# Optimization experiments

Hardware: AMD Instinct MI355X
Metric: run time of the kernel (lower is better)

Reference implementation:

```python
import jax, jax.numpy as jnp
import numpy as np

B, S, D, H = 4, 2048, 1024, 16
DK = D // H

def setup_inputs() -> dict:
    key = jax.random.key(0)
    ks = jax.random.split(key, 11)
    s = 1.0 / np.sqrt(D)
    return {
        "query": jax.random.normal(ks[0], (B, S, D), jnp.float32),
        "key": jax.random.normal(ks[1], (B, S, D), jnp.float32),
        "value": jax.random.normal(ks[2], (B, S, D), jnp.float32),
        "Wq_w": jax.random.normal(ks[3], (D, D), jnp.float32) * s,
        "Wq_b": jnp.zeros((D,), jnp.float32),
        "Wk_w": jax.random.normal(ks[4], (D, D), jnp.float32) * s,
        "Wk_b": jnp.zeros((D,), jnp.float32),
        "Wv_w": jax.random.normal(ks[5], (D, D), jnp.float32) * s,
        "Wv_b": jnp.zeros((D,), jnp.float32),
        "Wo_w": jax.random.normal(ks[6], (D, D), jnp.float32) * s,
        "Wo_b": jnp.zeros((D,), jnp.float32),
    }

def reference(query, key, value, Wq_w, Wq_b, Wk_w, Wk_b, Wv_w, Wv_b, Wo_w, Wo_b):
    b, s, d = query.shape
    # Linear projections (torch Linear: x @ W.T + b)
    q = query @ Wq_w.T + Wq_b
    k = key @ Wk_w.T + Wk_b
    v = value @ Wv_w.T + Wv_b
    # split heads -> [B, H, S, DK]
    q = q.reshape(b, s, H, DK).transpose(0, 2, 1, 3)
    k = k.reshape(b, s, H, DK).transpose(0, 2, 1, 3)
    v = v.reshape(b, s, H, DK).transpose(0, 2, 1, 3)
    # scaled dot-product attention
    scores = jnp.einsum("bhqd,bhkd->bhqk", q, k) / jnp.sqrt(jnp.asarray(DK, q.dtype))
    attn = jax.nn.softmax(scores, axis=-1)
    z = jnp.einsum("bhqk,bhkd->bhqd", attn, v)
    # merge heads and output projection
    z = z.transpose(0, 2, 1, 3).reshape(b, s, H * DK)
    return z @ Wo_w.T + Wo_b
```

## Files before the change

kernel.cpp:

```cpp
#include <hip/hip_runtime.h>
#include <stdint.h>

typedef unsigned short u16;
typedef __bf16 bf16x8 __attribute__((ext_vector_type(8)));
typedef float f32x4 __attribute__((ext_vector_type(4)));

#define B_   4
#define S_   2048
#define D_   1024
#define H_   16
#define DK_  64
#define MTOK (B_*S_)
#define LOG2E 1.4426950408889634f

static __device__ __forceinline__ float exp2_fast(float x){
  return __builtin_amdgcn_exp2f(x);
}

static __device__ __forceinline__ void gload_lds16(const void* g, void* l){
  __builtin_amdgcn_global_load_lds(
      (const __attribute__((address_space(1))) unsigned int*)g,
      (__attribute__((address_space(3))) unsigned int*)l, 16, 0, 0);
}

union bf8pack { __bf16 h[8]; uint4 u; };

__global__ void cvt4(const float* __restrict__ s0, const float* __restrict__ s1,
                     const float* __restrict__ s2, const float* __restrict__ s3,
                     u16* __restrict__ out, int n8){
  const float* s = blockIdx.y==0 ? s0 : blockIdx.y==1 ? s1 : blockIdx.y==2 ? s2 : s3;
  u16* o = out + (size_t)blockIdx.y * ((size_t)n8 * 8);
  int i = blockIdx.x * blockDim.x + threadIdx.x;
  int stride = gridDim.x * blockDim.x;
  for (; i < n8; i += stride){
    float4 v0 = reinterpret_cast<const float4*>(s)[i*2];
    float4 v1 = reinterpret_cast<const float4*>(s)[i*2+1];
    bf8pack p;
    p.h[0]=(__bf16)v0.x; p.h[1]=(__bf16)v0.y; p.h[2]=(__bf16)v0.z; p.h[3]=(__bf16)v0.w;
    p.h[4]=(__bf16)v1.x; p.h[5]=(__bf16)v1.y; p.h[6]=(__bf16)v1.z; p.h[7]=(__bf16)v1.w;
    reinterpret_cast<uint4*>(o)[i] = p.u;
  }
}

__global__ __launch_bounds__(256) void gemm_qkv(
    const float* __restrict__ q_in, const float* __restrict__ k_in, const float* __restrict__ v_in,
    const u16* __restrict__ wq, const u16* __restrict__ wk, const u16* __restrict__ wv,
    const float* __restrict__ bq, const float* __restrict__ bk, const float* __restrict__ bv,
    u16* __restrict__ Qb, u16* __restrict__ Kb, u16* __restrict__ VtG){
  const int z = blockIdx.z;
  const float* Ap   = z==0 ? q_in : z==1 ? k_in : v_in;
  const u16*   Bw   = z==0 ? wq : z==1 ? wk : wv;
  const float* bias = z==0 ? bq : z==1 ? bk : bv;
  const float scale = z==0 ? 0.125f*LOG2E : 1.0f;
  u16* Cb = z==0 ? Qb : z==1 ? Kb : VtG;

  __shared__ u16 As[2][128][32];
  __shared__ u16 Bs[2][128][32];
  const int tid  = threadIdx.x;
  const int lane = tid & 63;
  const int wid  = tid >> 6;
  const int wr = wid >> 1, wc = wid & 1;
  const int r15 = lane & 15, q4 = lane >> 4;
  const int bm = blockIdx.x, bn = blockIdx.y;
  const int K = D_, N = D_;
  const int NT = K / 32;

  const int r = tid >> 2, c = (tid & 3) << 3;
  const float* Ar0 = Ap + (size_t)(bm*128 + r)*K + c;
  const float* Ar1 = Ap + (size_t)(bm*128 + r + 64)*K + c;
  const u16*  Br0 = Bw + (size_t)(bn*128 + r)*K + c;
  const u16*  Br1 = Bw + (size_t)(bn*128 + r + 64)*K + c;

  f32x4 acc[4][4] = {};

  {
    float4 v00 = *reinterpret_cast<const float4*>(Ar0);
    float4 v01 = *reinterpret_cast<const float4*>(Ar0 + 4);
    float4 v10 = *reinterpret_cast<const float4*>(Ar1);
    float4 v11 = *reinterpret_cast<const float4*>(Ar1 + 4);
    bf8pack p0, p1;
    p0.h[0]=(__bf16)v00.x; p0.h[1]=(__bf16)v00.y; p0.h[2]=(__bf16)v00.z; p0.h[3]=(__bf16)v00.w;
    p0.h[4]=(__bf16)v01.x; p0.h[5]=(__bf16)v01.y; p0.h[6]=(__bf16)v01.z; p0.h[7]=(__bf16)v01.w;
    p1.h[0]=(__bf16)v10.x; p1.h[1]=(__bf16)v10.y; p1.h[2]=(__bf16)v10.z; p1.h[3]=(__bf16)v10.w;
    p1.h[4]=(__bf16)v11.x; p1.h[5]=(__bf16)v11.y; p1.h[6]=(__bf16)v11.z; p1.h[7]=(__bf16)v11.w;
    *reinterpret_cast<uint4*>(&As[0][r][c])    = p0.u;
    *reinterpret_cast<uint4*>(&As[0][r+64][c]) = p1.u;
    gload_lds16(Br0, &Bs[0][r][c]);
    gload_lds16(Br1, &Bs[0][r+64][c]);
  }
  __syncthreads();

  for (int t = 0; t < NT; ++t){
    const int cur = t & 1;
    float4 v00, v01, v10, v11;
    const bool pf = (t + 1 < NT);
    if (pf){
      const float* p0 = Ar0 + (t+1)*32;
      const float* p1 = Ar1 + (t+1)*32;
      v00 = *reinterpret_cast<const float4*>(p0);
      v01 = *reinterpret_cast<const float4*>(p0 + 4);
      v10 = *reinterpret_cast<const float4*>(p1);
      v11 = *reinterpret_cast<const float4*>(p1 + 4);
      gload_lds16(Br0 + (t+1)*32, &Bs[cur^1][r][c]);
      gload_lds16(Br1 + (t+1)*32, &Bs[cur^1][r+64][c]);
    }

    bf16x8 af[4], bfr[4];
    #pragma unroll
    for (int mf = 0; mf < 4; ++mf)
      af[mf] = *reinterpret_cast<const bf16x8*>(&As[cur][wr*64 + mf*16 + r15][q4*8]);
    #pragma unroll
    for (int nf = 0; nf < 4; ++nf)
      bfr[nf] = *reinterpret_cast<const bf16x8*>(&Bs[cur][wc*64 + nf*16 + r15][q4*8]);
    #pragma unroll
    for (int mf = 0; mf < 4; ++mf)
      #pragma unroll
      for (int nf = 0; nf < 4; ++nf)
        acc[mf][nf] = __builtin_amdgcn_mfma_f32_16x16x32_bf16(af[mf], bfr[nf], acc[mf][nf], 0, 0, 0);

    if (pf){
      bf8pack p0, p1;
      p0.h[0]=(__bf16)v00.x; p0.h[1]=(__bf16)v00.y; p0.h[2]=(__bf16)v00.z; p0.h[3]=(__bf16)v00.w;
      p0.h[4]=(__bf16)v01.x; p0.h[5]=(__bf16)v01.y; p0.h[6]=(__bf16)v01.z; p0.h[7]=(__bf16)v01.w;
      p1.h[0]=(__bf16)v10.x; p1.h[1]=(__bf16)v10.y; p1.h[2]=(__bf16)v10.z; p1.h[3]=(__bf16)v10.w;
      p1.h[4]=(__bf16)v11.x; p1.h[5]=(__bf16)v11.y; p1.h[6]=(__bf16)v11.z; p1.h[7]=(__bf16)v11.w;
      *reinterpret_cast<uint4*>(&As[cur^1][r][c])    = p0.u;
      *reinterpret_cast<uint4*>(&As[cur^1][r+64][c]) = p1.u;
    }
    __syncthreads();
  }

  #pragma unroll
  for (int nf = 0; nf < 4; ++nf){
    int col = bn*128 + wc*64 + nf*16 + r15;
    float bv = bias[col];
    if (z == 2){
      int h = col >> 6, dk = col & 63;
      #pragma unroll
      for (int mf = 0; mf < 4; ++mf){
        int row0 = bm*128 + wr*64 + mf*16 + q4*4;
        int bb = row0 >> 11, s0 = row0 & (S_-1);
        bf8pack p;
        #pragma unroll
        for (int j = 0; j < 4; ++j) p.h[j] = (__bf16)(acc[mf][nf][j] + bv);
        uint2 u; u.x = p.u.x; u.y = p.u.y;
        *reinterpret_cast<uint2*>(&Cb[((size_t)(bb*H_ + h)*DK_ + dk)*S_ + s0]) = u;
      }
    } else {
      #pragma unroll
      for (int mf = 0; mf < 4; ++mf){
        #pragma unroll
        for (int j = 0; j < 4; ++j){
          int row = bm*128 + wr*64 + mf*16 + q4*4 + j;
          __bf16 hv = (__bf16)((acc[mf][nf][j] + bv) * scale);
          Cb[(size_t)row*N + col] = *reinterpret_cast<u16*>(&hv);
        }
      }
    }
  }
}

__global__ __launch_bounds__(256) void gemm_out(const u16* __restrict__ Ab,
    const u16* __restrict__ Bw, const float* __restrict__ bias, float* __restrict__ Cf){
  __shared__ u16 As[2][128][32];
  __shared__ u16 Bs[2][128][32];
  const int tid  = threadIdx.x;
  const int lane = tid & 63;
  const int wid  = tid >> 6;
  const int wr = wid >> 1, wc = wid & 1;
  const int r15 = lane & 15, q4 = lane >> 4;
  const int bm = blockIdx.x, bn = blockIdx.y;
  const int K = D_, N = D_;
  const int NT = K / 32;

  const int r = tid >> 2, c = (tid & 3) << 3;
  const u16* Ar0 = Ab + (size_t)(bm*128 + r)*K + c;
  const u16* Ar1 = Ab + (size_t)(bm*128 + r + 64)*K + c;
  const u16* Br0 = Bw + (size_t)(bn*128 + r)*K + c;
  const u16* Br1 = Bw + (size_t)(bn*128 + r + 64)*K + c;

  f32x4 acc[4][4] = {};

  gload_lds16(Ar0, &As[0][r][c]);
  gload_lds16(Ar1, &As[0][r+64][c]);
  gload_lds16(Br0, &Bs[0][r][c]);
  gload_lds16(Br1, &Bs[0][r+64][c]);
  __syncthreads();

  for (int t = 0; t < NT; ++t){
    const int cur = t & 1;
    if (t + 1 < NT){
      gload_lds16(Ar0 + (t+1)*32, &As[cur^1][r][c]);
      gload_lds16(Ar1 + (t+1)*32, &As[cur^1][r+64][c]);
      gload_lds16(Br0 + (t+1)*32, &Bs[cur^1][r][c]);
      gload_lds16(Br1 + (t+1)*32, &Bs[cur^1][r+64][c]);
    }

    bf16x8 af[4], bfr[4];
    #pragma unroll
    for (int mf = 0; mf < 4; ++mf)
      af[mf] = *reinterpret_cast<const bf16x8*>(&As[cur][wr*64 + mf*16 + r15][q4*8]);
    #pragma unroll
    for (int nf = 0; nf < 4; ++nf)
      bfr[nf] = *reinterpret_cast<const bf16x8*>(&Bs[cur][wc*64 + nf*16 + r15][q4*8]);
    #pragma unroll
    for (int mf = 0; mf < 4; ++mf)
      #pragma unroll
      for (int nf = 0; nf < 4; ++nf)
        acc[mf][nf] = __builtin_amdgcn_mfma_f32_16x16x32_bf16(af[mf], bfr[nf], acc[mf][nf], 0, 0, 0);
    __syncthreads();
  }

  #pragma unroll
  for (int nf = 0; nf < 4; ++nf){
    int col = bn*128 + wc*64 + nf*16 + r15;
    float bv = bias[col];
    #pragma unroll
    for (int mf = 0; mf < 4; ++mf)
      #pragma unroll
      for (int j = 0; j < 4; ++j){
        int row = bm*128 + wr*64 + mf*16 + q4*4 + j;
        Cf[(size_t)row*N + col] = acc[mf][nf][j] + bv;
      }
  }
}

__global__ __launch_bounds__(256) void attn128(const u16* __restrict__ Qg,
    const u16* __restrict__ Kg, const u16* __restrict__ VtG, u16* __restrict__ Zg){
  __shared__ u16 Ks[64][72];
  __shared__ u16 Vts[64][72];
  __shared__ __bf16 Ps[128][68];
  const int tid  = threadIdx.x;
  const int lane = tid & 63;
  const int wv   = tid >> 6;
  const int r15  = lane & 15, q4 = lane >> 4;
  const int qt = blockIdx.x;
  const int bh = blockIdx.y;
  const int b = bh >> 4, h = bh & (H_-1);
  const size_t baseQ = ((size_t)b * S_) * D_ + (size_t)h * DK_;
  const size_t baseV = (size_t)bh * DK_ * S_;
  const int q0 = qt * 128;

  bf16x8 aq[2][2];
  #pragma unroll
  for (int mf = 0; mf < 2; ++mf){
    const u16* qr = Qg + baseQ + (size_t)(q0 + wv*32 + mf*16 + r15) * D_;
    aq[mf][0] = *reinterpret_cast<const bf16x8*>(qr + q4*8);
    aq[mf][1] = *reinterpret_cast<const bf16x8*>(qr + 32 + q4*8);
  }

  bf16x8 vones;
  #pragma unroll
  for (int i = 0; i < 8; ++i) vones[i] = (__bf16)1.0f;

  const int srow = tid >> 3, scol = (tid & 7) << 3;
  const u16* Kbase = Kg + baseQ;
  const u16* Vbase = VtG + baseV;

  uint4 kreg0, kreg1, vreg0, vreg1;
  kreg0 = *reinterpret_cast<const uint4*>(Kbase + (size_t)srow*D_ + scol);
  kreg1 = *reinterpret_cast<const uint4*>(Kbase + (size_t)(srow+32)*D_ + scol);
  vreg0 = *reinterpret_cast<const uint4*>(Vbase + (size_t)srow*S_ + scol);
  vreg1 = *reinterpret_cast<const uint4*>(Vbase + (size_t)(srow+32)*S_ + scol);

  f32x4 o_acc[2][4] = {};
  f32x4 l_acc[2] = {};

  for (int kt = 0; kt < S_/64; ++kt){
    if (kt) __syncthreads();
    *reinterpret_cast<uint4*>(&Ks[srow][scol])      = kreg0;
    *reinterpret_cast<uint4*>(&Ks[srow+32][scol])   = kreg1;
    *reinterpret_cast<uint4*>(&Vts[srow][scol])     = vreg0;
    *reinterpret_cast<uint4*>(&Vts[srow+32][scol])  = vreg1;
    __syncthreads();

    if (kt + 1 < S_/64){
      const u16* kp = Kbase + (size_t)((kt+1)*64 + srow)*D_ + scol;
      kreg0 = *reinterpret_cast<const uint4*>(kp);
      kreg1 = *reinterpret_cast<const uint4*>(kp + (size_t)32*D_);
      const u16* vp = Vbase + (size_t)srow*S_ + (kt+1)*64 + scol;
      vreg0 = *reinterpret_cast<const uint4*>(vp);
      vreg1 = *reinterpret_cast<const uint4*>(vp + (size_t)32*S_);
    }

    bf16x8 bk[4][2];
    #pragma unroll
    for (int nf = 0; nf < 4; ++nf){
      bk[nf][0] = *reinterpret_cast<const bf16x8*>(&Ks[nf*16 + r15][q4*8]);
      bk[nf][1] = *reinterpret_cast<const bf16x8*>(&Ks[nf*16 + r15][32 + q4*8]);
    }

    #pragma unroll
    for (int mf = 0; mf < 2; ++mf){
      f32x4 sacc[4] = {};
      #pragma unroll
      for (int nf = 0; nf < 4; ++nf){
        sacc[nf] = __builtin_amdgcn_mfma_f32_16x16x32_bf16(aq[mf][0], bk[nf][0], sacc[nf], 0, 0, 0);
        sacc[nf] = __builtin_amdgcn_mfma_f32_16x16x32_bf16(aq[mf][1], bk[nf][1], sacc[nf], 0, 0, 0);
      }
      #pragma unroll
      for (int nf = 0; nf < 4; ++nf)
        #pragma unroll
        for (int j = 0; j < 4; ++j)
          Ps[wv*32 + mf*16 + q4*4 + j][nf*16 + r15] = (__bf16)exp2_fast(sacc[nf][j]);
    }

    #pragma unroll
    for (int ks = 0; ks < 2; ++ks){
      bf16x8 bvf[4];
      #pragma unroll
      for (int nf = 0; nf < 4; ++nf)
        bvf[nf] = *reinterpret_cast<const bf16x8*>(&Vts[nf*16 + r15][ks*32 + q4*8]);
      #pragma unroll
      for (int mf = 0; mf < 2; ++mf){
        uint2 plo = *reinterpret_cast<const uint2*>(&Ps[wv*32 + mf*16 + r15][ks*32 + q4*8]);
        uint2 phi = *reinterpret_cast<const uint2*>(&Ps[wv*32 + mf*16 + r15][ks*32 + q4*8 + 4]);
        uint4 pw; pw.x = plo.x; pw.y = plo.y; pw.z = phi.x; pw.w = phi.y;
        bf16x8 ap = *reinterpret_cast<bf16x8*>(&pw);
        #pragma unroll
        for (int nf = 0; nf < 4; ++nf)
          o_acc[mf][nf] = __builtin_amdgcn_mfma_f32_16x16x32_bf16(ap, bvf[nf], o_acc[mf][nf], 0, 0, 0);
        l_acc[mf] = __builtin_amdgcn_mfma_f32_16x16x32_bf16(ap, vones, l_acc[mf], 0, 0, 0);
      }
    }
  }

  #pragma unroll
  for (int mf = 0; mf < 2; ++mf){
    f32x4 inv;
    #pragma unroll
    for (int j = 0; j < 4; ++j) inv[j] = 1.0f / l_acc[mf][j];
    #pragma unroll
    for (int nf = 0; nf < 4; ++nf)
      #pragma unroll
      for (int j = 0; j < 4; ++j){
        int qrw = q0 + wv*32 + mf*16 + q4*4 + j;
        int col = nf*16 + r15;
        __bf16 hv = (__bf16)(o_acc[mf][nf][j] * inv[j]);
        Zg[baseQ + (size_t)qrw*D_ + col] = *reinterpret_cast<u16*>(&hv);
      }
  }
}

extern "C" void kernel_launch(void* const* d_in, const int* in_sizes, int n_in,
                              void* d_out, int out_size, void* d_ws, size_t ws_size,
                              hipStream_t stream){
  const float* q_in = (const float*)d_in[0];
  const float* k_in = (const float*)d_in[1];
  const float* v_in = (const float*)d_in[2];
  const float* Wq_w = (const float*)d_in[3];
  const float* Wq_b = (const float*)d_in[4];
  const float* Wk_w = (const float*)d_in[5];
  const float* Wk_b = (const float*)d_in[6];
  const float* Wv_w = (const float*)d_in[7];
  const float* Wv_b = (const float*)d_in[8];
  const float* Wo_w = (const float*)d_in[9];
  const float* Wo_b = (const float*)d_in[10];
  float* out = (float*)d_out;

  u16* ws = (u16*)d_ws;
  const size_t WE = (size_t)D_ * D_;
  const size_t XE = (size_t)MTOK * D_;
  u16* wqb = ws;
  u16* wkb = wqb + WE;
  u16* wvb = wkb + WE;
  u16* wob = wvb + WE;
  u16* Qb  = wob + WE;
  u16* Kb  = Qb + XE;
  u16* VtG = Kb + XE;
  u16* Zb  = VtG + XE;

  cvt4<<<dim3(128, 4), 256, 0, stream>>>(Wq_w, Wk_w, Wv_w, Wo_w, wqb, (int)(WE/8));

  dim3 gqkv(MTOK/128, D_/128, 3), bb(256);
  gemm_qkv<<<gqkv, bb, 0, stream>>>(q_in, k_in, v_in, wqb, wkb, wvb,
                                    Wq_b, Wk_b, Wv_b, Qb, Kb, VtG);

  attn128<<<dim3(S_/128, B_*H_), bb, 0, stream>>>(Qb, Kb, VtG, Zb);

  gemm_out<<<dim3(MTOK/128, D_/128), bb, 0, stream>>>(Zb, wob, Wo_b, out);
}
```

Before: 224.1 us.

## Pre-convert activations to bf16 and remap attention blocks per XCD

Adds a conversion kernel that turns the fp32 query/key/value activations into bf16 in workspace before the QKV GEMM, when the workspace is large enough. The QKV GEMM can then stream both operands straight into LDS with global_load_lds, instead of loading fp32 through registers and converting in the inner loop. In exchange it writes and re-reads an extra bf16 copy of the activations. The attention launch becomes 1D, with a block-index remap that keeps the query tiles of the same heads on one XCD so K/V get more L2 reuse.

```diff
diff --git a/kernel.cpp b/kernel.cpp
--- a/kernel.cpp
+++ b/kernel.cpp
@@ -25,11 +25,41 @@
 
 union bf8pack { __bf16 h[8]; uint4 u; };
 
-__global__ void cvt4(const float* __restrict__ s0, const float* __restrict__ s1,
-                     const float* __restrict__ s2, const float* __restrict__ s3,
-                     u16* __restrict__ out, int n8){
-  const float* s = blockIdx.y==0 ? s0 : blockIdx.y==1 ? s1 : blockIdx.y==2 ? s2 : s3;
-  u16* o = out + (size_t)blockIdx.y * ((size_t)n8 * 8);
+#define COMPUTE(ASBUF, BSBUF) { \
+  bf16x8 af_[4], bf_[4]; \
+  _Pragma("unroll") \
+  for (int mf_ = 0; mf_ < 4; ++mf_) \
+    af_[mf_] = *reinterpret_cast<const bf16x8*>(&As[ASBUF][wr*64 + mf_*16 + r15][q4*8]); \
+  _Pragma("unroll") \
+  for (int nf_ = 0; nf_ < 4; ++nf_) \
+    bf_[nf_] = *reinterpret_cast<const bf16x8*>(&Bs[BSBUF][wc*64 + nf_*16 + r15][q4*8]); \
+  _Pragma("unroll") \
+  for (int mf_ = 0; mf_ < 4; ++mf_) \
+    _Pragma("unroll") \
+    for (int nf_ = 0; nf_ < 4; ++nf_) \
+      acc[mf_][nf_] = __builtin_amdgcn_mfma_f32_16x16x32_bf16(af_[mf_], bf_[nf_], acc[mf_][nf_], 0, 0, 0); }
+
+__global__ void cvt7(const float* __restrict__ q, const float* __restrict__ k,
+                     const float* __restrict__ v,
+                     const float* __restrict__ w0, const float* __restrict__ w1,
+                     const float* __restrict__ w2, const float* __restrict__ w3,
+                     u16* __restrict__ outW, u16* __restrict__ xq,
+                     u16* __restrict__ xk, u16* __restrict__ xv, int doAct){
+  const int y = blockIdx.y;
+  const float* s; u16* o; int n8;
+  const size_t WE = (size_t)D_ * D_;
+  const size_t XE = (size_t)MTOK * D_;
+  if (y < 3){
+    if (!doAct) return;
+    s = y==0 ? q : y==1 ? k : v;
+    o = y==0 ? xq : y==1 ? xk : xv;
+    n8 = (int)(XE/8);
+  } else {
+    int w = y - 3;
+    s = w==0 ? w0 : w==1 ? w1 : w==2 ? w2 : w3;
+    o = outW + (size_t)w * WE;
+    n8 = (int)(WE/8);
+  }
   int i = blockIdx.x * blockDim.x + threadIdx.x;
   int stride = gridDim.x * blockDim.x;
   for (; i < n8; i += stride){
@@ -42,7 +72,85 @@
   }
 }
 
-__global__ __launch_bounds__(256) void gemm_qkv(
+__global__ __launch_bounds__(256) void gemm_qkv2(
+    const u16* __restrict__ Xq, const u16* __restrict__ Xk, const u16* __restrict__ Xv,
+    const u16* __restrict__ wq, const u16* __restrict__ wk, const u16* __restrict__ wv,
+    const float* __restrict__ bq, const float* __restrict__ bk, const float* __restrict__ bv,
+    u16* __restrict__ Qb, u16* __restrict__ Kb, u16* __restrict__ VtG){
+  const int z = blockIdx.z;
+  const u16*   Ax   = z==0 ? Xq : z==1 ? Xk : Xv;
+  const u16*   Bw   = z==0 ? wq : z==1 ? wk : wv;
+  const float* bias = z==0 ? bq : z==1 ? bk : bv;
+  const float scale = z==0 ? 0.125f*LOG2E : 1.0f;
+  u16* Cb = z==0 ? Qb : z==1 ? Kb : VtG;
+
+  __shared__ u16 As[2][128][32];
+  __shared__ u16 Bs[2][128][32];
+  const int tid  = threadIdx.x;
+  const int lane = tid & 63;
+  const int wid  = tid >> 6;
+  const int wr = wid >> 1, wc = wid & 1;
+  const int r15 = lane & 15, q4 = lane >> 4;
+  const int bm = blockIdx.x, bn = blockIdx.y;
+  const int K = D_, N = D_;
+
+  const int r = tid >> 2, c = (tid & 3) << 3;
+  const u16* Aa0 = Ax + (size_t)(bm*128 + r)*K + c;
+  const u16* Aa1 = Ax + (size_t)(bm*128 + r + 64)*K + c;
+  const u16* Bb0 = Bw + (size_t)(bn*128 + r)*K + c;
+  const u16* Bb1 = Bw + (size_t)(bn*128 + r + 64)*K + c;
+
+  f32x4 acc[4][4] = {};
+
+  gload_lds16(Aa0, &As[0][r][c]);
+  gload_lds16(Aa1, &As[0][r+64][c]);
+  gload_lds16(Bb0, &Bs[0][r][c]);
+  gload_lds16(Bb1, &Bs[0][r+64][c]);
+  __syncthreads();
+
+  for (int t = 0; t < 32; ++t){
+    const int cur = t & 1;
+    if (t + 1 < 32){
+      gload_lds16(Aa0 + (size_t)(t+1)*32, &As[cur^1][r][c]);
+      gload_lds16(Aa1 + (size_t)(t+1)*32, &As[cur^1][r+64][c]);
+      gload_lds16(Bb0 + (size_t)(t+1)*32, &Bs[cur^1][r][c]);
+      gload_lds16(Bb1 + (size_t)(t+1)*32, &Bs[cur^1][r+64][c]);
+    }
+    COMPUTE(cur, cur);
+    __syncthreads();
+  }
+
+  #pragma unroll
+  for (int nf = 0; nf < 4; ++nf){
+    int col = bn*128 + wc*64 + nf*16 + r15;
+    float bv = bias[col];
+    if (z == 2){
+      int h = col >> 6, dk = col & 63;
+      #pragma unroll
+      for (int mf = 0; mf < 4; ++mf){
+        int row0 = bm*128 + wr*64 + mf*16 + q4*4;
+        int bb = row0 >> 11, sx = row0 & (S_-1);
+        bf8pack p;
+        #pragma unroll
+        for (int j = 0; j < 4; ++j) p.h[j] = (__bf16)(acc[mf][nf][j] + bv);
+        uint2 u; u.x = p.u.x; u.y = p.u.y;
+        *reinterpret_cast<uint2*>(&Cb[((size_t)(bb*H_ + h)*DK_ + dk)*S_ + sx]) = u;
+      }
+    } else {
+      #pragma unroll
+      for (int mf = 0; mf < 4; ++mf){
+        #pragma unroll
+        for (int j = 0; j < 4; ++j){
+          int row = bm*128 + wr*64 + mf*16 + q4*4 + j;
+          __bf16 hv = (__bf16)((acc[mf][nf][j] + bv) * scale);
+          Cb[(size_t)row*N + col] = *reinterpret_cast<u16*>(&hv);
+        }
+      }
+    }
+  }
+}
+
+__global__ __launch_bounds__(256) void gemm_qkv_reg(
     const float* __restrict__ q_in, const float* __restrict__ k_in, const float* __restrict__ v_in,
     const u16* __restrict__ wq, const u16* __restrict__ wk, const u16* __restrict__ wv,
     const float* __restrict__ bq, const float* __restrict__ bk, const float* __restrict__ bv,
@@ -63,21 +171,20 @@
   const int r15 = lane & 15, q4 = lane >> 4;
   const int bm = blockIdx.x, bn = blockIdx.y;
   const int K = D_, N = D_;
-  const int NT = K / 32;
 
   const int r = tid >> 2, c = (tid & 3) << 3;
-  const float* Ar0 = Ap + (size_t)(bm*128 + r)*K + c;
-  const float* Ar1 = Ap + (size_t)(bm*128 + r + 64)*K + c;
-  const u16*  Br0 = Bw + (size_t)(bn*128 + r)*K + c;
-  const u16*  Br1 = Bw + (size_t)(bn*128 + r + 64)*K + c;
+  const float* Ab0 = Ap + (size_t)(bm*128 + r)*K + c;
+  const float* Ab1 = Ap + (size_t)(bm*128 + r + 64)*K + c;
+  const u16*  Bb0 = Bw + (size_t)(bn*128 + r)*K + c;
+  const u16*  Bb1 = Bw + (size_t)(bn*128 + r + 64)*K + c;
 
   f32x4 acc[4][4] = {};
 
   {
-    float4 v00 = *reinterpret_cast<const float4*>(Ar0);
-    float4 v01 = *reinterpret_cast<const float4*>(Ar0 + 4);
-    float4 v10 = *reinterpret_cast<const float4*>(Ar1);
-    float4 v11 = *reinterpret_cast<const float4*>(Ar1 + 4);
+    float4 v00 = *reinterpret_cast<const float4*>(Ab0);
+    float4 v01 = *reinterpret_cast<const float4*>(Ab0 + 4);
+    float4 v10 = *reinterpret_cast<const float4*>(Ab1);
+    float4 v11 = *reinterpret_cast<const float4*>(Ab1 + 4);
     bf8pack p0, p1;
     p0.h[0]=(__bf16)v00.x; p0.h[1]=(__bf16)v00.y; p0.h[2]=(__bf16)v00.z; p0.h[3]=(__bf16)v00.w;
     p0.h[4]=(__bf16)v01.x; p0.h[5]=(__bf16)v01.y; p0.h[6]=(__bf16)v01.z; p0.h[7]=(__bf16)v01.w;
@@ -85,39 +192,26 @@
     p1.h[4]=(__bf16)v11.x; p1.h[5]=(__bf16)v11.y; p1.h[6]=(__bf16)v11.z; p1.h[7]=(__bf16)v11.w;
     *reinterpret_cast<uint4*>(&As[0][r][c])    = p0.u;
     *reinterpret_cast<uint4*>(&As[0][r+64][c]) = p1.u;
-    gload_lds16(Br0, &Bs[0][r][c]);
-    gload_lds16(Br1, &Bs[0][r+64][c]);
+    gload_lds16(Bb0, &Bs[0][r][c]);
+    gload_lds16(Bb1, &Bs[0][r+64][c]);
   }
   __syncthreads();
 
-  for (int t = 0; t < NT; ++t){
+  for (int t = 0; t < 32; ++t){
     const int cur = t & 1;
     float4 v00, v01, v10, v11;
-    const bool pf = (t + 1 < NT);
+    const bool pf = (t + 1 < 32);
     if (pf){
-      const float* p0 = Ar0 + (t+1)*32;
-      const float* p1 = Ar1 + (t+1)*32;
+      const float* p0 = Ab0 + (size_t)(t+1)*32;
+      const float* p1 = Ab1 + (size_t)(t+1)*32;
       v00 = *reinterpret_cast<const float4*>(p0);
       v01 = *reinterpret_cast<const float4*>(p0 + 4);
       v10 = *reinterpret_cast<const float4*>(p1);
       v11 = *reinterpret_cast<const float4*>(p1 + 4);
-      gload_lds16(Br0 + (t+1)*32, &Bs[cur^1][r][c]);
-      gload_lds16(Br1 + (t+1)*32, &Bs[cur^1][r+64][c]);
-    }
-
-    bf16x8 af[4], bfr[4];
-    #pragma unroll
-    for (int mf = 0; mf < 4; ++mf)
-      af[mf] = *reinterpret_cast<const bf16x8*>(&As[cur][wr*64 + mf*16 + r15][q4*8]);
-    #pragma unroll
-    for (int nf = 0; nf < 4; ++nf)
-      bfr[nf] = *reinterpret_cast<const bf16x8*>(&Bs[cur][wc*64 + nf*16 + r15][q4*8]);
-    #pragma unroll
-    for (int mf = 0; mf < 4; ++mf)
-      #pragma unroll
-      for (int nf = 0; nf < 4; ++nf)
-        acc[mf][nf] = __builtin_amdgcn_mfma_f32_16x16x32_bf16(af[mf], bfr[nf], acc[mf][nf], 0, 0, 0);
-
+      gload_lds16(Bb0 + (size_t)(t+1)*32, &Bs[cur^1][r][c]);
+      gload_lds16(Bb1 + (size_t)(t+1)*32, &Bs[cur^1][r+64][c]);
+    }
+    COMPUTE(cur, cur);
     if (pf){
       bf8pack p0, p1;
       p0.h[0]=(__bf16)v00.x; p0.h[1]=(__bf16)v00.y; p0.h[2]=(__bf16)v00.z; p0.h[3]=(__bf16)v00.w;
@@ -139,12 +233,12 @@
       #pragma unroll
       for (int mf = 0; mf < 4; ++mf){
         int row0 = bm*128 + wr*64 + mf*16 + q4*4;
-        int bb = row0 >> 11, s0 = row0 & (S_-1);
+        int bb = row0 >> 11, sx = row0 & (S_-1);
         bf8pack p;
         #pragma unroll
         for (int j = 0; j < 4; ++j) p.h[j] = (__bf16)(acc[mf][nf][j] + bv);
         uint2 u; u.x = p.u.x; u.y = p.u.y;
-        *reinterpret_cast<uint2*>(&Cb[((size_t)(bb*H_ + h)*DK_ + dk)*S_ + s0]) = u;
+        *reinterpret_cast<uint2*>(&Cb[((size_t)(bb*H_ + h)*DK_ + dk)*S_ + sx]) = u;
       }
     } else {
       #pragma unroll
@@ -171,43 +265,30 @@
   const int r15 = lane & 15, q4 = lane >> 4;
   const int bm = blockIdx.x, bn = blockIdx.y;
   const int K = D_, N = D_;
-  const int NT = K / 32;
 
   const int r = tid >> 2, c = (tid & 3) << 3;
-  const u16* Ar0 = Ab + (size_t)(bm*128 + r)*K + c;
-  const u16* Ar1 = Ab + (size_t)(bm*128 + r + 64)*K + c;
-  const u16* Br0 = Bw + (size_t)(bn*128 + r)*K + c;
-  const u16* Br1 = Bw + (size_t)(bn*128 + r + 64)*K + c;
+  const u16* Aa0 = Ab + (size_t)(bm*128 + r)*K + c;
+  const u16* Aa1 = Ab + (size_t)(bm*128 + r + 64)*K + c;
+  const u16* Bb0 = Bw + (size_t)(bn*128 + r)*K + c;
+  const u16* Bb1 = Bw + (size_t)(bn*128 + r + 64)*K + c;
 
   f32x4 acc[4][4] = {};
 
-  gload_lds16(Ar0, &As[0][r][c]);
-  gload_lds16(Ar1, &As[0][r+64][c]);
-  gload_lds16(Br0, &Bs[0][r][c]);
-  gload_lds16(Br1, &Bs[0][r+64][c]);
+  gload_lds16(Aa0, &As[0][r][c]);
+  gload_lds16(Aa1, &As[0][r+64][c]);
+  gload_lds16(Bb0, &Bs[0][r][c]);
+  gload_lds16(Bb1, &Bs[0][r+64][c]);
   __syncthreads();
 
-  for (int t = 0; t < NT; ++t){
+  for (int t = 0; t < 32; ++t){
     const int cur = t & 1;
-    if (t + 1 < NT){
-      gload_lds16(Ar0 + (t+1)*32, &As[cur^1][r][c]);
-      gload_lds16(Ar1 + (t+1)*32, &As[cur^1][r+64][c]);
-      gload_lds16(Br0 + (t+1)*32, &Bs[cur^1][r][c]);
-      gload_lds16(Br1 + (t+1)*32, &Bs[cur^1][r+64][c]);
-    }
-
-    bf16x8 af[4], bfr[4];
-    #pragma unroll
-    for (int mf = 0; mf < 4; ++mf)
-      af[mf] = *reinterpret_cast<const bf16x8*>(&As[cur][wr*64 + mf*16 + r15][q4*8]);
-    #pragma unroll
-    for (int nf = 0; nf < 4; ++nf)
-      bfr[nf] = *reinterpret_cast<const bf16x8*>(&Bs[cur][wc*64 + nf*16 + r15][q4*8]);
-    #pragma unroll
-    for (int mf = 0; mf < 4; ++mf)
-      #pragma unroll
-      for (int nf = 0; nf < 4; ++nf)
-        acc[mf][nf] = __builtin_amdgcn_mfma_f32_16x16x32_bf16(af[mf], bfr[nf], acc[mf][nf], 0, 0, 0);
+    if (t + 1 < 32){
+      gload_lds16(Aa0 + (size_t)(t+1)*32, &As[cur^1][r][c]);
+      gload_lds16(Aa1 + (size_t)(t+1)*32, &As[cur^1][r+64][c]);
+      gload_lds16(Bb0 + (size_t)(t+1)*32, &Bs[cur^1][r][c]);
+      gload_lds16(Bb1 + (size_t)(t+1)*32, &Bs[cur^1][r+64][c]);
+    }
+    COMPUTE(cur, cur);
     __syncthreads();
   }
 
@@ -234,8 +315,10 @@
   const int lane = tid & 63;
   const int wv   = tid >> 6;
   const int r15  = lane & 15, q4 = lane >> 4;
-  const int qt = blockIdx.x;
-  const int bh = blockIdx.y;
+  const int bid = blockIdx.x;
+  const int xcd = bid & 7, ii = bid >> 3;
+  const int bh = xcd*8 + (ii >> 4);
+  const int qt = ii & 15;
   const int b = bh >> 4, h = bh & (H_-1);
   const size_t baseQ = ((size_t)b * S_) * D_ + (size_t)h * DK_;
   const size_t baseV = (size_t)bh * DK_ * S_;
@@ -369,14 +452,26 @@
   u16* Kb  = Qb + XE;
   u16* VtG = Kb + XE;
   u16* Zb  = VtG + XE;
-
-  cvt4<<<dim3(128, 4), 256, 0, stream>>>(Wq_w, Wk_w, Wv_w, Wo_w, wqb, (int)(WE/8));
+  u16* Xq  = Zb;
+  u16* Xk  = Zb + XE;
+  u16* Xv  = Xk + XE;
+
+  const size_t NEED = (4*WE + 6*XE) * sizeof(u16);
+  const int big = (ws_size >= NEED) ? 1 : 0;
+
+  cvt7<<<dim3(512, 7), 256, 0, stream>>>(q_in, k_in, v_in,
+                                         Wq_w, Wk_w, Wv_w, Wo_w,
+                                         wqb, Xq, Xk, Xv, big);
 
   dim3 gqkv(MTOK/128, D_/128, 3), bb(256);
-  gemm_qkv<<<gqkv, bb, 0, stream>>>(q_in, k_in, v_in, wqb, wkb, wvb,
-                                    Wq_b, Wk_b, Wv_b, Qb, Kb, VtG);
-
-  attn128<<<dim3(S_/128, B_*H_), bb, 0, stream>>>(Qb, Kb, VtG, Zb);
+  if (big)
+    gemm_qkv2<<<gqkv, bb, 0, stream>>>(Xq, Xk, Xv, wqb, wkb, wvb,
+                                       Wq_b, Wk_b, Wv_b, Qb, Kb, VtG);
+  else
+    gemm_qkv_reg<<<gqkv, bb, 0, stream>>>(q_in, k_in, v_in, wqb, wkb, wvb,
+                                          Wq_b, Wk_b, Wv_b, Qb, Kb, VtG);
+
+  attn128<<<dim3(B_*H_*(S_/128)), bb, 0, stream>>>(Qb, Kb, VtG, Zb);
 
   gemm_out<<<dim3(MTOK/128, D_/128), bb, 0, stream>>>(Zb, wob, Wo_b, out);
 }
```

Result: slower. 234.5 us (+4.6%).
